# Kernel optimization log

Measured on AMD Instinct MI355X. Metric: run time of the kernel, lower is better.

## Reference

```python
import jax, jax.numpy as jnp
import numpy as np
import math

B, DIM, H, W = 4, 96, 64, 64
DIM3 = DIM * 3
DSTATE = 16

def _dwconv(x, w, b):
    # x: (B, d, L); torch Conv1d(k=4, pad=3, groups=d) then slice [:L] == left-pad 3
    y = jax.lax.conv_general_dilated(x, w, (1,), [(3, 0)],
                                     dimension_numbers=('NCH', 'OIH', 'NCH'),
                                     feature_group_count=x.shape[1])
    return y + b[None, :, None]

def _ln(x, g, b):
    m = jnp.mean(x, -1, keepdims=True)
    v = jnp.var(x, -1, keepdims=True)
    return (x - m) * jax.lax.rsqrt(v + 1e-5) * g + b

def _selective_scan(u, delta, A, Bs, Cs, D, z, delta_bias):
    # u, delta, z: (B, d, L); A: (d, N); Bs, Cs: (B, N, L)
    delta = jax.nn.softplus(delta + delta_bias[None, :, None])
    dT, uT = jnp.moveaxis(delta, 2, 0), jnp.moveaxis(u, 2, 0)   # (L, B, d)
    BT, CT = jnp.moveaxis(Bs, 2, 0), jnp.moveaxis(Cs, 2, 0)     # (L, B, N)
    h0 = jnp.zeros((u.shape[0], A.shape[0], A.shape[1]), u.dtype)
    def step(h, inp):
        d_t, u_t, b_t, c_t = inp
        h = jnp.exp(d_t[..., None] * A) * h + (d_t * u_t)[..., None] * b_t[:, None, :]
        return h, jnp.einsum('bdn,bn->bd', h, c_t)
    _, ys = jax.lax.scan(step, h0, (dT, uT, BT, CT))
    y = jnp.moveaxis(ys, 0, 2) + D[None, :, None] * u
    return y * jax.nn.silu(z)

def _sss(x, z_anchor, in_w, conv_w, conv_b, x_w, dt_w, dt_b, Alog, Dp, out_w):
    Bb, C, Hh, Ww = x.shape
    L = Hh * Ww
    r = dt_w.shape[0]
    xf = x.reshape(Bb, C, L).transpose(0, 2, 1) + z_anchor[:, None, :]
    x_in, z_gate = jnp.split(xf @ in_w, 2, axis=-1)
    xc = jax.nn.silu(_dwconv(x_in.transpose(0, 2, 1), conv_w, conv_b))  # (B, di, L)
    xdbl = xc.transpose(0, 2, 1) @ x_w
    dt, Bs, Cs = jnp.split(xdbl, [r, r + DSTATE], axis=-1)
    y = _selective_scan(xc, (dt @ dt_w).transpose(0, 2, 1), -jnp.exp(Alog),
                        Bs.transpose(0, 2, 1), Cs.transpose(0, 2, 1), Dp,
                        z_gate.transpose(0, 2, 1), dt_b)
    return (y.transpose(0, 2, 1) @ out_w).transpose(0, 2, 1).reshape(Bb, C, Hh, Ww)

def _sts(x, K, Q, in_w, conv_w, conv_b, kln_g, kln_b, k_w, k_b, qln_g, qln_b, q_w, q_b,
         dtbc_w, dt_w, dt_b, gate_w, gate_b, Alog, Dp, out_w):
    Bb, C, Hh, Ww = x.shape
    L = Hh * Ww
    r = dt_w.shape[0]
    xf = x.reshape(Bb, C, L).transpose(0, 2, 1)
    xc = jax.nn.silu(_dwconv((xf @ in_w).transpose(0, 2, 1), conv_w, conv_b))  # (B, di, L)
    x_t = xc.transpose(0, 2, 1)
    Kf = K.reshape(Bb, C, L).transpose(0, 2, 1)
    Qf = Q.reshape(Bb, C, L).transpose(0, 2, 1)
    K_p = jax.nn.silu(_ln(Kf, kln_g, kln_b) @ k_w + k_b)
    Q_p = jax.nn.silu(_ln(Qf, qln_g, qln_b) @ q_w + q_b)
    xdbl = jnp.concatenate([x_t, K_p], -1) @ dtbc_w
    dt, Bs, Cs = jnp.split(xdbl, [r, r + DSTATE], axis=-1)
    z_g = (jnp.concatenate([x_t, Q_p], -1) @ gate_w + gate_b).transpose(0, 2, 1)
    y = _selective_scan(xc, (dt @ dt_w).transpose(0, 2, 1), -jnp.exp(Alog),
                        Bs.transpose(0, 2, 1), Cs.transpose(0, 2, 1), Dp, z_g, dt_b)
    return (y.transpose(0, 2, 1) @ out_w).transpose(0, 2, 1).reshape(Bb, C, Hh, Ww)

def setup_inputs():
    key = jax.random.key(0)
    ks = iter(jax.random.split(key, 64))
    def nrm(shape, s=0.02):
        return jax.random.normal(next(ks), shape, jnp.float32) * s
    di, di3 = DIM * 2, DIM3 * 2
    r, r3 = math.ceil(DIM / 16), math.ceil(DIM3 / 16)
    Alog = jnp.log(jnp.tile(jnp.arange(1.0, DSTATE + 1.0, dtype=jnp.float32), (di, 1)))
    Alog3 = jnp.log(jnp.tile(jnp.arange(1.0, DSTATE + 1.0, dtype=jnp.float32), (di3, 1)))
    return dict(
        m_ll=jax.random.normal(next(ks), (B, DIM, H, W), jnp.float32),
        m_high=jax.random.normal(next(ks), (B, DIM3, H, W), jnp.float32),
        z=jax.random.normal(next(ks), (B, DIM), jnp.float32),
        K=jax.random.normal(next(ks), (B, DIM3, H, W), jnp.float32),
        Q=jax.random.normal(next(ks), (B, DIM3, H, W), jnp.float32),
        s_in_w=nrm((DIM, 2 * di)), s_conv_w=nrm((di, 1, 4), 0.2), s_conv_b=nrm((di,)),
        s_x_w=nrm((di, r + 2 * DSTATE)), s_dt_w=nrm((r, di)), s_dt_b=nrm((di,)),
        s_Alog=Alog, s_D=jnp.ones((di,), jnp.float32), s_out_w=nrm((di, DIM)),
        t_in_w=nrm((DIM3, di3)), t_conv_w=nrm((di3, 1, 4), 0.2), t_conv_b=nrm((di3,)),
        t_kln_g=jnp.ones((DIM3,), jnp.float32), t_kln_b=jnp.zeros((DIM3,), jnp.float32),
        t_k_w=nrm((DIM3, di3)), t_k_b=nrm((di3,)),
        t_qln_g=jnp.ones((DIM3,), jnp.float32), t_qln_b=jnp.zeros((DIM3,), jnp.float32),
        t_q_w=nrm((DIM3, di3)), t_q_b=nrm((di3,)),
        t_dtbc_w=nrm((2 * di3, r3 + 2 * DSTATE)), t_dt_w=nrm((r3, di3)), t_dt_b=nrm((di3,)),
        t_gate_w=nrm((2 * di3, di3)), t_gate_b=nrm((di3,)),
        t_Alog=Alog3, t_D=jnp.ones((di3,), jnp.float32), t_out_w=nrm((di3, DIM3)),
    )

def reference(m_ll, m_high, z, K, Q,
              s_in_w, s_conv_w, s_conv_b, s_x_w, s_dt_w, s_dt_b, s_Alog, s_D, s_out_w,
              t_in_w, t_conv_w, t_conv_b, t_kln_g, t_kln_b, t_k_w, t_k_b,
              t_qln_g, t_qln_b, t_q_w, t_q_b, t_dtbc_w, t_dt_w, t_dt_b,
              t_gate_w, t_gate_b, t_Alog, t_D, t_out_w):
    o1 = m_ll + _sss(m_ll, z, s_in_w, s_conv_w, s_conv_b, s_x_w, s_dt_w, s_dt_b, s_Alog, s_D, s_out_w)
    o2 = m_high + _sts(m_high, K, Q, t_in_w, t_conv_w, t_conv_b, t_kln_g, t_kln_b, t_k_w, t_k_b,
                       t_qln_g, t_qln_b, t_q_w, t_q_b, t_dtbc_w, t_dt_w, t_dt_b,
                       t_gate_w, t_gate_b, t_Alog, t_D, t_out_w)
    return (o1, o2)
```

## Files before the change

### kernel.cpp

```cpp
#include <hip/hip_runtime.h>
#include <math.h>

#define L 4096

typedef unsigned short u16;
typedef unsigned int u32;
typedef float f32x4 __attribute__((ext_vector_type(4)));
typedef short s16x8 __attribute__((ext_vector_type(8)));
typedef __attribute__((address_space(3))) unsigned int lds_u32;
typedef __attribute__((address_space(1))) unsigned int glb_u32;

__device__ __forceinline__ float softplus_f(float x) {
  return fmaxf(x, 0.f) + log1pf(__expf(-fabsf(x)));
}
__device__ __forceinline__ float silu_f(float x) {
  return x / (1.f + __expf(-x));
}
__device__ __forceinline__ float bf2f(u16 v) {
  return __uint_as_float(((unsigned)v) << 16);
}
__device__ __forceinline__ u16 f2bf(float f) {
  unsigned u = __float_as_uint(f);
  u += 0x7FFFu + ((u >> 16) & 1u);
  return (u16)(u >> 16);
}

struct WSeg { const float* src; u16* dst; int K, N, Npad; };
struct WAll { WSeg s[8]; };

__global__ __launch_bounds__(256) void wconv_k(WAll wa) {
  const WSeg w = wa.s[blockIdx.z];
  const int nb = blockIdx.x * 32, kb = blockIdx.y * 32;
  if (nb >= w.Npad || kb >= w.K) return;
  __shared__ float t[32][33];
  const int tx = threadIdx.x & 31, ty = threadIdx.x >> 5;
  for (int r = ty; r < 32; r += 8) {
    int k = kb + r, n = nb + tx;
    t[r][tx] = (n < w.N) ? w.src[(size_t)k * w.N + n] : 0.f;
  }
  __syncthreads();
  for (int r = ty; r < 32; r += 8) {
    int n = nb + r;
    w.dst[(size_t)n * w.K + kb + tx] = f2bf(t[tx][r]);
  }
}

struct TSeg { const float *x, *gam, *bet, *bias2; u16* out; int C, doLN; };
struct TPack { TSeg s[4]; };

__global__ __launch_bounds__(256) void trans_pack_k(TPack pk) {
  const TSeg t = pk.s[blockIdx.x >> 9];
  const int local = blockIdx.x & 511;
  const int C = t.C;
  __shared__ float tile[288][33];
  __shared__ float psum[8][32], psq[8][32];
  __shared__ float mm[32], rr[32];
  const int tid = threadIdx.x;
  const int l0 = (local & 127) * 32;
  const int b = local >> 7;
  const int lane32 = tid & 31, row8 = tid >> 5;
  const float* xb = t.x + (size_t)b * C * L + l0;

  for (int c = row8; c < C; c += 8)
    tile[c][lane32] = xb[(size_t)c * L + lane32];
  __syncthreads();

  if (t.doLN) {
    float s = 0.f, sq = 0.f;
    for (int c = row8; c < C; c += 8) {
      float v = tile[c][lane32];
      s += v; sq = fmaf(v, v, sq);
    }
    psum[row8][lane32] = s; psq[row8][lane32] = sq;
    __syncthreads();
    if (row8 == 0) {
      float ts = 0.f, tq = 0.f;
      #pragma unroll
      for (int g = 0; g < 8; ++g) { ts += psum[g][lane32]; tq += psq[g][lane32]; }
      float m = ts / C;
      float var = tq / C - m * m;
      mm[lane32] = m;
      rr[lane32] = rsqrtf(var + 1e-5f);
    }
    __syncthreads();
  }

  u16* ob = t.out + ((size_t)b * L + l0) * C;
  const int total = 32 * C;
  for (int o = tid * 8; o < total; o += 2048) {
    int tt = o / C, c = o % C;
    float m = 0.f, rs = 0.f;
    if (t.doLN) { m = mm[tt]; rs = rr[tt]; }
    union { u16 u[8]; int4 v; } pkv;
    #pragma unroll
    for (int j = 0; j < 8; ++j) {
      float v = tile[c + j][tt];
      if (t.doLN) v = (v - m) * rs * t.gam[c + j] + t.bet[c + j];
      else if (t.bias2) v += t.bias2[b * C + c + j];
      pkv.u[j] = f2bf(v);
    }
    *(int4*)(ob + o) = pkv.v;
  }
}

struct CSeg { const u16* x; const float* w; const float* b; u16* y; int C, nbx; };
struct CPack { CSeg s[2]; int start1; };

__global__ __launch_bounds__(256) void conv_pack_k(CPack pk) {
  const int bid = blockIdx.x;
  const int si = bid >= pk.start1;
  const CSeg q = pk.s[si];
  const int local = si ? bid - pk.start1 : bid;
  const int C = q.C;
  const int c = (local % q.nbx) * 64 + (threadIdx.x & 63);
  const int chunk = (local / q.nbx) * 4 + (threadIdx.x >> 6);
  const int T0 = chunk * 8;
  const float w0 = q.w[c * 4], w1 = q.w[c * 4 + 1], w2 = q.w[c * 4 + 2], w3 = q.w[c * 4 + 3];
  const float bs = q.b[c];
  const bool first = (T0 & (L - 1)) == 0;
  float v[11];
  #pragma unroll
  for (int i = 0; i < 11; ++i) {
    if (i < 3 && first) v[i] = 0.f;
    else v[i] = bf2f(q.x[(size_t)(T0 - 3 + i) * C + c]);
  }
  #pragma unroll
  for (int j = 0; j < 8; ++j) {
    float s = bs + w0 * v[j] + w1 * v[j + 1] + w2 * v[j + 2] + w3 * v[j + 3];
    q.y[(size_t)(T0 + j) * C + c] = f2bf(silu_f(s));
  }
}

struct MSeg {
  const u16 *A0, *A1, *Wt;
  const float *bias, *res;
  float* outF; u16 *outB0, *outB1;
  int K, K1, Nout, ldA, ldo, split, nbx, nwg, epi;
};
struct MPack { MSeg s[4]; int starts[4]; int nseg; };

__global__ __launch_bounds__(256) void mfma_pack_k(MPack pk) {
  const int bid = blockIdx.x;
  int si = 0;
  #pragma unroll
  for (int k = 1; k < 4; ++k)
    if (k < pk.nseg && bid >= pk.starts[k]) si = k;
  const MSeg p = pk.s[si];
  const int wg = bid - pk.starts[si];

  __shared__ u16 lds[16384];
  u16* As0 = lds;
  u16* Bs0 = lds + 8192;
  const int tid = threadIdx.x;
  const int lane = tid & 63;
  const int wid = tid >> 6;
  const int wm = wid >> 1, wn = wid & 1;
  const int newid = (wg & 7) * (p.nwg >> 3) + (wg >> 3);
  const int n0 = (newid % p.nbx) * 128;
  const int m0 = (newid / p.nbx) * 128;
  const int srow = tid & 127;
  const int skc = tid >> 7;
  const int kgrp = lane >> 4, l16 = lane & 15;

  f32x4 acc[4][4];
  #pragma unroll
  for (int i = 0; i < 4; ++i)
    #pragma unroll
    for (int j = 0; j < 4; ++j)
      acc[i][j] = (f32x4){0.f, 0.f, 0.f, 0.f};

  auto stage = [&](int bi, int k0) {
    const u16* Ab = p.A0;
    int kc = k0;
    if (p.A1 && k0 >= p.K1) { Ab = p.A1; kc = k0 - p.K1; }
    const u16* g0 = Ab + (size_t)(m0 + srow) * p.ldA + kc + skc * 8;
    u16* Ad = As0 + bi * 4096;
    __builtin_amdgcn_global_load_lds((const glb_u32*)g0,
        (lds_u32*)(Ad + wid * 512), 16, 0, 0);
    __builtin_amdgcn_global_load_lds((const glb_u32*)(g0 + 16),
        (lds_u32*)(Ad + 2048 + wid * 512), 16, 0, 0);
    const u16* h0 = p.Wt + (size_t)(n0 + srow) * p.K + k0 + skc * 8;
    u16* Bd = Bs0 + bi * 4096;
    __builtin_amdgcn_global_load_lds((const glb_u32*)h0,
        (lds_u32*)(Bd + wid * 512), 16, 0, 0);
    __builtin_amdgcn_global_load_lds((const glb_u32*)(h0 + 16),
        (lds_u32*)(Bd + 2048 + wid * 512), 16, 0, 0);
  };

  const int nt = p.K >> 5;
  stage(0, 0);
  __syncthreads();
  for (int t = 0; t < nt; ++t) {
    const int cur = t & 1;
    if (t + 1 < nt) stage(cur ^ 1, (t + 1) << 5);
    s16x8 af[4], bfr[4];
    #pragma unroll
    for (int mi = 0; mi < 4; ++mi)
      af[mi] = *(const s16x8*)(As0 + cur * 4096 + kgrp * 1024 + (wm * 64 + mi * 16 + l16) * 8);
    #pragma unroll
    for (int ni = 0; ni < 4; ++ni)
      bfr[ni] = *(const s16x8*)(Bs0 + cur * 4096 + kgrp * 1024 + (wn * 64 + ni * 16 + l16) * 8);
    #pragma unroll
    for (int mi = 0; mi < 4; ++mi)
      #pragma unroll
      for (int ni = 0; ni < 4; ++ni)
        acc[mi][ni] = __builtin_amdgcn_mfma_f32_16x16x32_bf16(af[mi], bfr[ni], acc[mi][ni], 0, 0, 0);
    if (t + 1 < nt) __syncthreads();
  }

  if (p.epi == 0) {
    #pragma unroll
    for (int mi = 0; mi < 4; ++mi) {
      #pragma unroll
      for (int j = 0; j < 4; ++j) {
        int token = m0 + wm * 64 + mi * 16 + (lane >> 4) * 4 + j;
        #pragma unroll
        for (int ni = 0; ni < 4; ++ni) {
          int n = n0 + wn * 64 + ni * 16 + l16;
          if (n < p.Nout) p.outF[(size_t)token * p.ldo + n] = acc[mi][ni][j];
        }
      }
    }
  } else if (p.epi == 2) {
    #pragma unroll
    for (int mi = 0; mi < 4; ++mi) {
      int token = m0 + wm * 64 + mi * 16 + (lane >> 4) * 4;
      int b = token >> 12, l = token & (L - 1);
      #pragma unroll
      for (int ni = 0; ni < 4; ++ni) {
        int n = n0 + wn * 64 + ni * 16 + l16;
        if (n < p.Nout) {
          size_t o = ((size_t)b * p.Nout + n) * L + l;
          float4 r = *(const float4*)(p.res + o);
          float4 v = make_float4(acc[mi][ni][0] + r.x, acc[mi][ni][1] + r.y,
                                 acc[mi][ni][2] + r.z, acc[mi][ni][3] + r.w);
          *(float4*)(p.outF + o) = v;
        }
      }
    }
  } else {
    __syncthreads();
    #pragma unroll
    for (int mi = 0; mi < 4; ++mi) {
      #pragma unroll
      for (int j = 0; j < 4; ++j) {
        int tok = wm * 64 + mi * 16 + (lane >> 4) * 4 + j;
        #pragma unroll
        for (int ni = 0; ni < 4; ++ni) {
          int nl = wn * 64 + ni * 16 + l16;
          int n = n0 + nl;
          float v = acc[mi][ni][j];
          if (n < p.Nout && (p.epi == 3 || p.epi == 4)) {
            v += p.bias[n];
            if (p.epi == 3) v = silu_f(v);
          }
          lds[tok * 128 + ((((nl >> 4) ^ (tok & 7))) << 4) + (nl & 15)] = f2bf(v);
        }
      }
    }
    __syncthreads();
    #pragma unroll
    for (int it = 0; it < 8; ++it) {
      int idx = it * 256 + tid;
      int row = idx >> 4, c16 = idx & 15;
      int nl0 = c16 * 8;
      if (n0 + nl0 < p.Nout) {
        int g = nl0 >> 4;
        int4 vv = *(const int4*)(lds + row * 128 + ((g ^ (row & 7)) << 4) + (nl0 & 15));
        int token = m0 + row;
        if (p.epi == 5) {
          int n = n0 + nl0;
          if (n < p.split) *(int4*)(p.outB0 + (size_t)token * p.split + n) = vv;
          else *(int4*)(p.outB1 + (size_t)token * p.split + (n - p.split)) = vv;
        } else {
          *(int4*)(p.outB0 + (size_t)token * p.ldo + n0 + nl0) = vv;
        }
      }
    }
  }
}

struct FSeg { const float* A0; const float* W; const float* eb; float* out; int K, N, lda, ldo, nbx; };
struct FPack { FSeg s[2]; int start1; };

__global__ __launch_bounds__(256) void gemm_f32_pack_k(FPack pk) {
  const int bid = blockIdx.x;
  const int si = bid >= pk.start1;
  const FSeg p = pk.s[si];
  const int local = si ? bid - pk.start1 : bid;
  const int n0 = (local % p.nbx) * 64;
  const int m0 = (local / p.nbx) * 64;

  __shared__ __align__(16) float As[16][64];
  __shared__ __align__(16) float Bs[16][64];
  const int tid = threadIdx.x;
  const int kidx = tid >> 4;
  const int li4 = (tid & 15) << 2;
  const int r0 = (tid & 15) << 2;
  const int c0 = (tid >> 4) << 2;
  float acc[4][4] = {};

  for (int k0 = 0; k0 < p.K; k0 += 16) {
    __syncthreads();
    {
      const int row = tid >> 2;
      const int kk4 = (tid & 3) << 2;
      const float* src = p.A0 + (size_t)(m0 + row) * p.lda;
      #pragma unroll
      for (int j = 0; j < 4; ++j) {
        int k = k0 + kk4 + j;
        As[kk4 + j][row] = (k < p.K) ? src[k] : 0.f;
      }
    }
    {
      int k = k0 + kidx;
      #pragma unroll
      for (int j = 0; j < 4; ++j) {
        int n = n0 + li4 + j;
        Bs[kidx][li4 + j] = (k < p.K && n < p.N) ? p.W[(size_t)k * p.N + n] : 0.f;
      }
    }
    __syncthreads();
    #pragma unroll
    for (int kk = 0; kk < 16; ++kk) {
      float4 a = *(const float4*)&As[kk][r0];
      float4 bq = *(const float4*)&Bs[kk][c0];
      float av[4] = {a.x, a.y, a.z, a.w};
      float bv[4] = {bq.x, bq.y, bq.z, bq.w};
      #pragma unroll
      for (int i = 0; i < 4; ++i)
        #pragma unroll
        for (int j = 0; j < 4; ++j)
          acc[i][j] = fmaf(av[i], bv[j], acc[i][j]);
    }
  }
  float eb[4] = {p.eb[n0 + c0], p.eb[n0 + c0 + 1], p.eb[n0 + c0 + 2], p.eb[n0 + c0 + 3]};
  #pragma unroll
  for (int i = 0; i < 4; ++i) {
    float4 v;
    v.x = softplus_f(acc[i][0] + eb[0]);
    v.y = softplus_f(acc[i][1] + eb[1]);
    v.z = softplus_f(acc[i][2] + eb[2]);
    v.w = softplus_f(acc[i][3] + eb[3]);
    *(float4*)&p.out[(size_t)(m0 + r0 + i) * p.ldo + n0 + c0] = v;
  }
}

struct S3Seg {
  const u16* u; const float* dlt; const float* Alog; const float* xdbl;
  const float* Dp; const u16* zT; float* PF; u16* yT;
  int roff, Dch, CLen, NCH, nsl;
};
struct S3Pack { S3Seg s[2]; int start1; };

template<int PASS>
__global__ __launch_bounds__(256) void scan3_pack_k(S3Pack pk) {
  __shared__ float rows[64][32];
  const int bid = blockIdx.x;
  const int si = bid >= pk.start1;
  const S3Seg q = pk.s[si];
  const int local = si ? bid - pk.start1 : bid;
  const int nsl = q.nsl;
  const int NC = L / q.CLen;
  const int slice = local % nsl;
  const int c = (local / nsl) % NC;
  const int b = local / (nsl * NC);
  const int tid = threadIdx.x;
  const size_t tok0 = (size_t)b * L + (size_t)c * q.CLen;

  const int W2 = (PASS == 1) ? 8 : 16;
  const int tot2 = q.CLen * W2;
  for (int i = tid; i < tot2; i += 256) {
    int r = i / W2, j = i - r * W2;
    float2 v = *(const float2*)(q.xdbl + (tok0 + r) * 64 + q.roff + 2 * j);
    *(float2*)&rows[r][2 * j] = v;
  }
  __syncthreads();

  if (tid < 192) {
    const int d = slice * 192 + tid;
    const int Dch = q.Dch;
    float An[16], h[16];
    #pragma unroll
    for (int n = 0; n < 16; ++n) {
      An[n] = -__expf(q.Alog[d * 16 + n]);
      h[n] = 0.f;
    }
    bool fast = true;
    #pragma unroll
    for (int n = 1; n < 16; ++n) {
      float ref = (float)(n + 1) * An[0];
      if (fabsf(An[n] - ref) > 1e-4f * fabsf(ref)) fast = false;
    }
    const int ch = b * Dch + d;
    if (PASS == 3) {
      #pragma unroll
      for (int n = 0; n < 16; ++n)
        h[n] = q.PF[((size_t)c * 32 + 16 + n) * q.NCH + ch];
    }
    const float Dd = q.Dp[d];
    const u16* up = q.u + tok0 * Dch + d;
    const float* dp = q.dlt + tok0 * Dch + d;
    const u16* zp = q.zT + tok0 * Dch + d;
    u16* yr = q.yT + tok0 * Dch + d;
    float S = 0.f;

    float dl_n = dp[0];
    float uu_n = bf2f(up[0]);
    float zv_n = (PASS == 3) ? bf2f(zp[0]) : 0.f;

    #define SCAN_BODY(FAST)                                                    \
    for (int t = 0; t < q.CLen; ++t) {                                         \
      float dl = dl_n, uu = uu_n, zv = zv_n;                                   \
      if (t + 1 < q.CLen) {                                                    \
        const size_t on = (size_t)(t + 1) * Dch;                               \
        dl_n = dp[on];                                                         \
        uu_n = bf2f(up[on]);                                                   \
        if (PASS == 3) zv_n = bf2f(zp[on]);                                    \
      }                                                                        \
      float w = dl * uu;                                                       \
      f32x4 B4[4];                                                             \
      _Pragma("unroll")                                                        \
      for (int g = 0; g < 4; ++g) B4[g] = *(const f32x4*)&rows[t][4 * g];      \
      if (PASS == 1) S += dl;                                                  \
      if (FAST) {                                                              \
        float a = __expf(dl * An[0]);                                          \
        float e[16];                                                           \
        e[0] = a;                                                              \
        e[1] = a * a;                                                          \
        e[2] = e[1] * e[0];                                                    \
        e[3] = e[1] * e[1];                                                    \
        e[4] = e[3] * e[0]; e[5] = e[3] * e[1];                                \
        e[6] = e[3] * e[2]; e[7] = e[3] * e[3];                                \
        _Pragma("unroll")                                                      \
        for (int j2 = 0; j2 < 8; ++j2) e[8 + j2] = e[7] * e[j2];               \
        _Pragma("unroll")                                                      \
        for (int n = 0; n < 16; ++n)                                           \
          h[n] = fmaf(e[n], h[n], w * B4[n >> 2][n & 3]);                      \
      } else {                                                                 \
        _Pragma("unroll")                                                      \
        for (int n = 0; n < 16; ++n)                                           \
          h[n] = fmaf(__expf(dl * An[n]), h[n], w * B4[n >> 2][n & 3]);        \
      }                                                                        \
      if (PASS == 3) {                                                         \
        f32x4 C4[4];                                                           \
        _Pragma("unroll")                                                      \
        for (int g = 0; g < 4; ++g) C4[g] = *(const f32x4*)&rows[t][16 + 4 * g]; \
        float y0 = 0.f, y1 = 0.f, y2 = 0.f, y3 = 0.f;                          \
        _Pragma("unroll")                                                      \
        for (int k2 = 0; k2 < 4; ++k2) {                                       \
          y0 = fmaf(h[k2],      C4[0][k2], y0);                                \
          y1 = fmaf(h[4 + k2],  C4[1][k2], y1);                                \
          y2 = fmaf(h[8 + k2],  C4[2][k2], y2);                                \
          y3 = fmaf(h[12 + k2], C4[3][k2], y3);                                \
        }                                                                      \
        float y = (y0 + y1) + (y2 + y3);                                       \
        yr[(size_t)t * Dch] = f2bf((y + Dd * uu) * silu_f(zv));                \
      }                                                                        \
    }

    if (fast) { SCAN_BODY(1) } else { SCAN_BODY(0) }
    #undef SCAN_BODY

    if (PASS == 1) {
      #pragma unroll
      for (int n = 0; n < 16; ++n) {
        q.PF[((size_t)c * 32 + n) * q.NCH + ch] = __expf(An[n] * S);
        q.PF[((size_t)c * 32 + 16 + n) * q.NCH + ch] = h[n];
      }
    }
  }
}

__global__ __launch_bounds__(256) void stitch_pack_k(
    float* PF0, int NC0, int NCH0, int tot0,
    float* PF1, int NC1, int NCH1, int tot1) {
  int idx = blockIdx.x * 256 + threadIdx.x;
  float* PF; int NC, NCH;
  if (idx < tot0) { PF = PF0; NC = NC0; NCH = NCH0; }
  else { idx -= tot0; if (idx >= tot1) return; PF = PF1; NC = NC1; NCH = NCH1; }
  int ch = idx % NCH, n = idx / NCH;
  float hin = 0.f;
  for (int c = 0; c < NC; ++c) {
    float* Ps = PF + ((size_t)c * 32 + n) * NCH + ch;
    float* Fs = PF + ((size_t)c * 32 + 16 + n) * NCH + ch;
    float Pv = *Ps, Fv = *Fs;
    *Fs = hin;
    hin = fmaf(Pv, hin, Fv);
  }
}

extern "C" void kernel_launch(void* const* d_in, const int* in_sizes, int n_in,
                              void* d_out, int out_size, void* d_ws, size_t ws_size,
                              hipStream_t stream) {
  const float* m_ll    = (const float*)d_in[0];
  const float* m_high  = (const float*)d_in[1];
  const float* zanc    = (const float*)d_in[2];
  const float* Kin     = (const float*)d_in[3];
  const float* Qin     = (const float*)d_in[4];
  const float* s_in_w  = (const float*)d_in[5];
  const float* s_conv_w= (const float*)d_in[6];
  const float* s_conv_b= (const float*)d_in[7];
  const float* s_x_w   = (const float*)d_in[8];
  const float* s_dt_w  = (const float*)d_in[9];
  const float* s_dt_b  = (const float*)d_in[10];
  const float* s_Alog  = (const float*)d_in[11];
  const float* s_D     = (const float*)d_in[12];
  const float* s_out_w = (const float*)d_in[13];
  const float* t_in_w  = (const float*)d_in[14];
  const float* t_conv_w= (const float*)d_in[15];
  const float* t_conv_b= (const float*)d_in[16];
  const float* t_kln_g = (const float*)d_in[17];
  const float* t_kln_b = (const float*)d_in[18];
  const float* t_k_w   = (const float*)d_in[19];
  const float* t_k_b   = (const float*)d_in[20];
  const float* t_qln_g = (const float*)d_in[21];
  const float* t_qln_b = (const float*)d_in[22];
  const float* t_q_w   = (const float*)d_in[23];
  const float* t_q_b   = (const float*)d_in[24];
  const float* t_dtbc_w= (const float*)d_in[25];
  const float* t_dt_w  = (const float*)d_in[26];
  const float* t_dt_b  = (const float*)d_in[27];
  const float* t_gate_w= (const float*)d_in[28];
  const float* t_gate_b= (const float*)d_in[29];
  const float* t_Alog  = (const float*)d_in[30];
  const float* t_D     = (const float*)d_in[31];
  const float* t_out_w = (const float*)d_in[32];

  float* out1 = (float*)d_out;
  float* out2 = out1 + (size_t)4 * 96 * L;
  float* ws = (float*)d_ws;

  u16* w_sin   = (u16*)(ws + 0);
  u16* w_sx    = (u16*)(ws + 18432);
  u16* w_sout  = (u16*)(ws + 30720);
  u16* w_tin   = (u16*)(ws + 43008);
  u16* w_tk    = (u16*)(ws + 135168);
  u16* w_tq    = (u16*)(ws + 227328);
  u16* w_tdtbc = (u16*)(ws + 319488);
  u16* w_tgate = (u16*)(ws + 393216);
  u16* w_tout  = (u16*)(ws + 761856);

  float* B_ahi  = ws + 872448;
  float* B_aK   = ws + 3231744;
  float* B_aQ   = ws + 5591040;
  float* B_all  = ws + 7950336;
  float* B_xin  = ws + 8736768;
  float* B_zTs  = ws + 10309632;
  float* B_xc   = ws + 11882496;
  float* B_xin3 = ws + 13455360;
  float* B_xc3  = ws + 18173952;
  float* B_kp   = ws + 22892544;
  float* B_qp   = ws + 27611136;
  float* B_zg3  = ws + 32329728;
  float* B_xdbl = ws + 37048320;
  float* B_xdbl3= ws + 38096896;
  float* B_PFs  = ws + 39145472;
  float* B_dlt  = B_ahi;
  float* B_dlt3 = B_kp;
  u16* y_bf = (u16*)B_xin;
  u16* y3   = (u16*)B_xin3;
  float* PFt = out2;

  dim3 blk(256);

  {
    WAll wa;
    wa.s[0] = {s_in_w,   w_sin,    96, 384, 384};
    wa.s[1] = {s_x_w,    w_sx,    192,  38, 128};
    wa.s[2] = {s_out_w,  w_sout,  192,  96, 128};
    wa.s[3] = {t_in_w,   w_tin,   288, 576, 640};
    wa.s[4] = {t_k_w,    w_tk,    288, 576, 640};
    wa.s[5] = {t_q_w,    w_tq,    288, 576, 640};
    wa.s[6] = {t_dtbc_w, w_tdtbc, 1152, 50, 128};
    wa.s[7] = {t_gate_w, w_tgate, 1152, 576, 640};
    wconv_k<<<dim3(20, 36, 8), blk, 0, stream>>>(wa);
    WAll wb;
    wb.s[0] = {t_out_w,  w_tout,  576, 288, 384};
    wconv_k<<<dim3(12, 18, 1), blk, 0, stream>>>(wb);
  }

  {
    TPack tp{};
    tp.s[0] = {m_ll,   nullptr, nullptr, zanc,    (u16*)B_all, 96,  0};
    tp.s[1] = {m_high, nullptr, nullptr, nullptr, (u16*)B_ahi, 288, 0};
    tp.s[2] = {Kin,    t_kln_g, t_kln_b, nullptr, (u16*)B_aK,  288, 1};
    tp.s[3] = {Qin,    t_qln_g, t_qln_b, nullptr, (u16*)B_aQ,  288, 1};
    trans_pack_k<<<dim3(2048), blk, 0, stream>>>(tp);
  }

  {
    MPack pk{}; pk.nseg = 4;
    pk.starts[0] = 0; pk.starts[1] = 384; pk.starts[2] = 1024; pk.starts[3] = 1664;
    MSeg a{}; a.A0 = (u16*)B_all; a.Wt = w_sin; a.K = 96; a.K1 = 1 << 28; a.Nout = 384;
    a.ldA = 96; a.split = 192; a.outB0 = (u16*)B_xin; a.outB1 = (u16*)B_zTs;
    a.nbx = 3; a.nwg = 384; a.epi = 5; pk.s[0] = a;
    MSeg b{}; b.A0 = (u16*)B_ahi; b.Wt = w_tin; b.K = 288; b.K1 = 1 << 28; b.Nout = 576;
    b.ldA = 288; b.ldo = 576; b.outB0 = (u16*)B_xin3; b.nbx = 5; b.nwg = 640; b.epi = 1; pk.s[1] = b;
    MSeg c{}; c.A0 = (u16*)B_aK; c.Wt = w_tk; c.K = 288; c.K1 = 1 << 28; c.Nout = 576;
    c.ldA = 288; c.ldo = 576; c.bias = t_k_b; c.outB0 = (u16*)B_kp; c.nbx = 5; c.nwg = 640; c.epi = 3; pk.s[2] = c;
    MSeg d{}; d.A0 = (u16*)B_aQ; d.Wt = w_tq; d.K = 288; d.K1 = 1 << 28; d.Nout = 576;
    d.ldA = 288; d.ldo = 576; d.bias = t_q_b; d.outB0 = (u16*)B_qp; d.nbx = 5; d.nwg = 640; d.epi = 3; pk.s[3] = d;
    mfma_pack_k<<<dim3(2304), blk, 0, stream>>>(pk);
  }

  {
    CPack cp{}; cp.start1 = 1536;
    cp.s[0] = {(u16*)B_xin,  s_conv_w, s_conv_b, (u16*)B_xc,  192, 3};
    cp.s[1] = {(u16*)B_xin3, t_conv_w, t_conv_b, (u16*)B_xc3, 576, 9};
    conv_pack_k<<<dim3(6144), blk, 0, stream>>>(cp);
  }

  {
    MPack pk{}; pk.nseg = 3;
    pk.starts[0] = 0; pk.starts[1] = 128; pk.starts[2] = 256; pk.starts[3] = 896;
    MSeg a{}; a.A0 = (u16*)B_xc; a.Wt = w_sx; a.K = 192; a.K1 = 1 << 28; a.Nout = 64;
    a.ldA = 192; a.ldo = 64; a.outF = B_xdbl; a.nbx = 1; a.nwg = 128; a.epi = 0; pk.s[0] = a;
    MSeg b{}; b.A0 = (u16*)B_xc3; b.A1 = (u16*)B_kp; b.Wt = w_tdtbc; b.K = 1152; b.K1 = 576;
    b.Nout = 64; b.ldA = 576; b.ldo = 64; b.outF = B_xdbl3; b.nbx = 1; b.nwg = 128; b.epi = 0; pk.s[1] = b;
    MSeg c{}; c.A0 = (u16*)B_xc3; c.A1 = (u16*)B_qp; c.Wt = w_tgate; c.K = 1152; c.K1 = 576;
    c.Nout = 576; c.ldA = 576; c.ldo = 576; c.bias = t_gate_b; c.outB0 = (u16*)B_zg3;
    c.nbx = 5; c.nwg = 640; c.epi = 4; pk.s[2] = c;
    mfma_pack_k<<<dim3(896), blk, 0, stream>>>(pk);
  }

  {
    FPack fp{}; fp.start1 = 768;
    fp.s[0] = {B_xdbl,  s_dt_w, s_dt_b, B_dlt,  6,  192, 64, 192, 3};
    fp.s[1] = {B_xdbl3, t_dt_w, t_dt_b, B_dlt3, 18, 576, 64, 576, 9};
    gemm_f32_pack_k<<<dim3(3072), blk, 0, stream>>>(fp);
  }

  S3Pack sp{}; sp.start1 = 512;
  sp.s[0] = {(u16*)B_xc,  B_dlt,  s_Alog, B_xdbl,  s_D, (u16*)B_zTs, B_PFs, y_bf, 6,  192, 32, 768,  1};
  sp.s[1] = {(u16*)B_xc3, B_dlt3, t_Alog, B_xdbl3, t_D, (u16*)B_zg3, PFt,   y3,   18, 576, 64, 2304, 3};
  scan3_pack_k<1><<<dim3(1280), blk, 0, stream>>>(sp);
  stitch_pack_k<<<dim3(192), blk, 0, stream>>>(B_PFs, 128, 768, 12288, PFt, 64, 2304, 36864);
  scan3_pack_k<3><<<dim3(1280), blk, 0, stream>>>(sp);

  {
    MPack pk{}; pk.nseg = 2;
    pk.starts[0] = 0; pk.starts[1] = 128; pk.starts[2] = 512; pk.starts[3] = 512;
    MSeg a{}; a.A0 = y_bf; a.Wt = w_sout; a.K = 192; a.K1 = 1 << 28; a.Nout = 96;
    a.ldA = 192; a.res = m_ll; a.outF = out1; a.nbx = 1; a.nwg = 128; a.epi = 2; pk.s[0] = a;
    MSeg b{}; b.A0 = y3; b.Wt = w_tout; b.K = 576; b.K1 = 1 << 28; b.Nout = 288;
    b.ldA = 576; b.res = m_high; b.outF = out2; b.nbx = 3; b.nwg = 384; b.epi = 2; pk.s[1] = b;
    mfma_pack_k<<<dim3(512), blk, 0, stream>>>(pk);
  }
}
```

Baseline: 408.8 us.

## Fuse dt projection and softplus into the selective scan kernels

Removes the separate fp32 GEMM that computed delta = softplus(dt @ dt_w + dt_b) into a full (tokens x channels) fp32 buffer. Each scan pass now stages the dt rows in LDS and recomputes delta per timestep with an 18-term dot product against per-thread weights held in registers. This removes one kernel launch plus the write and two reads of a large fp32 delta tensor. In exchange it adds register pressure and redundant arithmetic, since delta is computed in both scan passes.

```diff
diff --git a/kernel.cpp b/kernel.cpp
--- a/kernel.cpp
+++ b/kernel.cpp
@@ -280,82 +280,18 @@
   }
 }
 
-struct FSeg { const float* A0; const float* W; const float* eb; float* out; int K, N, lda, ldo, nbx; };
-struct FPack { FSeg s[2]; int start1; };
-
-__global__ __launch_bounds__(256) void gemm_f32_pack_k(FPack pk) {
-  const int bid = blockIdx.x;
-  const int si = bid >= pk.start1;
-  const FSeg p = pk.s[si];
-  const int local = si ? bid - pk.start1 : bid;
-  const int n0 = (local % p.nbx) * 64;
-  const int m0 = (local / p.nbx) * 64;
-
-  __shared__ __align__(16) float As[16][64];
-  __shared__ __align__(16) float Bs[16][64];
-  const int tid = threadIdx.x;
-  const int kidx = tid >> 4;
-  const int li4 = (tid & 15) << 2;
-  const int r0 = (tid & 15) << 2;
-  const int c0 = (tid >> 4) << 2;
-  float acc[4][4] = {};
-
-  for (int k0 = 0; k0 < p.K; k0 += 16) {
-    __syncthreads();
-    {
-      const int row = tid >> 2;
-      const int kk4 = (tid & 3) << 2;
-      const float* src = p.A0 + (size_t)(m0 + row) * p.lda;
-      #pragma unroll
-      for (int j = 0; j < 4; ++j) {
-        int k = k0 + kk4 + j;
-        As[kk4 + j][row] = (k < p.K) ? src[k] : 0.f;
-      }
-    }
-    {
-      int k = k0 + kidx;
-      #pragma unroll
-      for (int j = 0; j < 4; ++j) {
-        int n = n0 + li4 + j;
-        Bs[kidx][li4 + j] = (k < p.K && n < p.N) ? p.W[(size_t)k * p.N + n] : 0.f;
-      }
-    }
-    __syncthreads();
-    #pragma unroll
-    for (int kk = 0; kk < 16; ++kk) {
-      float4 a = *(const float4*)&As[kk][r0];
-      float4 bq = *(const float4*)&Bs[kk][c0];
-      float av[4] = {a.x, a.y, a.z, a.w};
-      float bv[4] = {bq.x, bq.y, bq.z, bq.w};
-      #pragma unroll
-      for (int i = 0; i < 4; ++i)
-        #pragma unroll
-        for (int j = 0; j < 4; ++j)
-          acc[i][j] = fmaf(av[i], bv[j], acc[i][j]);
-    }
-  }
-  float eb[4] = {p.eb[n0 + c0], p.eb[n0 + c0 + 1], p.eb[n0 + c0 + 2], p.eb[n0 + c0 + 3]};
-  #pragma unroll
-  for (int i = 0; i < 4; ++i) {
-    float4 v;
-    v.x = softplus_f(acc[i][0] + eb[0]);
-    v.y = softplus_f(acc[i][1] + eb[1]);
-    v.z = softplus_f(acc[i][2] + eb[2]);
-    v.w = softplus_f(acc[i][3] + eb[3]);
-    *(float4*)&p.out[(size_t)(m0 + r0 + i) * p.ldo + n0 + c0] = v;
-  }
-}
-
 struct S3Seg {
-  const u16* u; const float* dlt; const float* Alog; const float* xdbl;
+  const u16* u; const float* Alog; const float* xdbl;
+  const float* dtw; const float* dtb;
   const float* Dp; const u16* zT; float* PF; u16* yT;
-  int roff, Dch, CLen, NCH, nsl;
+  int rdim, Dch, CLen, NCH, nsl;
 };
 struct S3Pack { S3Seg s[2]; int start1; };
 
 template<int PASS>
 __global__ __launch_bounds__(256) void scan3_pack_k(S3Pack pk) {
-  __shared__ float rows[64][32];
+  __shared__ float rows_bc[64][32];
+  __shared__ float rows_dt[64][18];
   const int bid = blockIdx.x;
   const int si = bid >= pk.start1;
   const S3Seg q = pk.s[si];
@@ -368,12 +304,20 @@
   const int tid = threadIdx.x;
   const size_t tok0 = (size_t)b * L + (size_t)c * q.CLen;
 
-  const int W2 = (PASS == 1) ? 8 : 16;
-  const int tot2 = q.CLen * W2;
-  for (int i = tid; i < tot2; i += 256) {
-    int r = i / W2, j = i - r * W2;
-    float2 v = *(const float2*)(q.xdbl + (tok0 + r) * 64 + q.roff + 2 * j);
-    *(float2*)&rows[r][2 * j] = v;
+  {
+    const int W2 = (PASS == 1) ? 8 : 16;
+    const int tot2 = q.CLen * W2;
+    for (int i = tid; i < tot2; i += 256) {
+      int r = i / W2, j = i - r * W2;
+      float2 v = *(const float2*)(q.xdbl + (tok0 + r) * 64 + q.rdim + 2 * j);
+      *(float2*)&rows_bc[r][2 * j] = v;
+    }
+    const int totd = q.CLen * 9;
+    for (int i = tid; i < totd; i += 256) {
+      int r = i / 9, j = i - r * 9;
+      float2 v = *(const float2*)(q.xdbl + (tok0 + r) * 64 + 2 * j);
+      *(float2*)&rows_dt[r][2 * j] = v;
+    }
   }
   __syncthreads();
 
@@ -392,6 +336,12 @@
       float ref = (float)(n + 1) * An[0];
       if (fabsf(An[n] - ref) > 1e-4f * fabsf(ref)) fast = false;
     }
+    float wc[18];
+    #pragma unroll
+    for (int k = 0; k < 18; ++k)
+      wc[k] = (k < q.rdim) ? q.dtw[k * Dch + d] : 0.f;
+    const float db = q.dtb[d];
+
     const int ch = b * Dch + d;
     if (PASS == 3) {
       #pragma unroll
@@ -400,12 +350,21 @@
     }
     const float Dd = q.Dp[d];
     const u16* up = q.u + tok0 * Dch + d;
-    const float* dp = q.dlt + tok0 * Dch + d;
     const u16* zp = q.zT + tok0 * Dch + d;
     u16* yr = q.yT + tok0 * Dch + d;
     float S = 0.f;
 
-    float dl_n = dp[0];
+    auto dlt_at = [&](int t) {
+      float a0 = db, a1 = 0.f;
+      #pragma unroll
+      for (int k = 0; k < 9; ++k) {
+        a0 = fmaf(rows_dt[t][2 * k], wc[2 * k], a0);
+        a1 = fmaf(rows_dt[t][2 * k + 1], wc[2 * k + 1], a1);
+      }
+      return softplus_f(a0 + a1);
+    };
+
+    float dl_n = dlt_at(0);
     float uu_n = bf2f(up[0]);
     float zv_n = (PASS == 3) ? bf2f(zp[0]) : 0.f;
 
@@ -414,14 +373,14 @@
       float dl = dl_n, uu = uu_n, zv = zv_n;                                   \
       if (t + 1 < q.CLen) {                                                    \
         const size_t on = (size_t)(t + 1) * Dch;                               \
-        dl_n = dp[on];                                                         \
+        dl_n = dlt_at(t + 1);                                                  \
         uu_n = bf2f(up[on]);                                                   \
         if (PASS == 3) zv_n = bf2f(zp[on]);                                    \
       }                                                                        \
       float w = dl * uu;                                                       \
       f32x4 B4[4];                                                             \
       _Pragma("unroll")                                                        \
-      for (int g = 0; g < 4; ++g) B4[g] = *(const f32x4*)&rows[t][4 * g];      \
+      for (int g = 0; g < 4; ++g) B4[g] = *(const f32x4*)&rows_bc[t][4 * g];   \
       if (PASS == 1) S += dl;                                                  \
       if (FAST) {                                                              \
         float a = __expf(dl * An[0]);                                          \
@@ -445,7 +404,7 @@
       if (PASS == 3) {                                                         \
         f32x4 C4[4];                                                           \
         _Pragma("unroll")                                                      \
-        for (int g = 0; g < 4; ++g) C4[g] = *(const f32x4*)&rows[t][16 + 4 * g]; \
+        for (int g = 0; g < 4; ++g) C4[g] = *(const f32x4*)&rows_bc[t][16 + 4 * g]; \
         float y0 = 0.f, y1 = 0.f, y2 = 0.f, y3 = 0.f;                          \
         _Pragma("unroll")                                                      \
         for (int k2 = 0; k2 < 4; ++k2) {                                       \
@@ -556,8 +515,6 @@
   float* B_xdbl = ws + 37048320;
   float* B_xdbl3= ws + 38096896;
   float* B_PFs  = ws + 39145472;
-  float* B_dlt  = B_ahi;
-  float* B_dlt3 = B_kp;
   u16* y_bf = (u16*)B_xin;
   u16* y3   = (u16*)B_xin3;
   float* PFt = out2;
@@ -624,16 +581,9 @@
     mfma_pack_k<<<dim3(896), blk, 0, stream>>>(pk);
   }
 
-  {
-    FPack fp{}; fp.start1 = 768;
-    fp.s[0] = {B_xdbl,  s_dt_w, s_dt_b, B_dlt,  6,  192, 64, 192, 3};
-    fp.s[1] = {B_xdbl3, t_dt_w, t_dt_b, B_dlt3, 18, 576, 64, 576, 9};
-    gemm_f32_pack_k<<<dim3(3072), blk, 0, stream>>>(fp);
-  }
-
   S3Pack sp{}; sp.start1 = 512;
-  sp.s[0] = {(u16*)B_xc,  B_dlt,  s_Alog, B_xdbl,  s_D, (u16*)B_zTs, B_PFs, y_bf, 6,  192, 32, 768,  1};
-  sp.s[1] = {(u16*)B_xc3, B_dlt3, t_Alog, B_xdbl3, t_D, (u16*)B_zg3, PFt,   y3,   18, 576, 64, 2304, 3};
+  sp.s[0] = {(u16*)B_xc,  s_Alog, B_xdbl,  s_dt_w, s_dt_b, s_D, (u16*)B_zTs, B_PFs, y_bf, 6,  192, 32, 768,  1};
+  sp.s[1] = {(u16*)B_xc3, t_Alog, B_xdbl3, t_dt_w, t_dt_b, t_D, (u16*)B_zg3, PFt,   y3,   18, 576, 64, 2304, 3};
   scan3_pack_k<1><<<dim3(1280), blk, 0, stream>>>(sp);
   stitch_pack_k<<<dim3(192), blk, 0, stream>>>(B_PFs, 128, 768, 12288, PFt, 64, 2304, 36864);
   scan3_pack_k<3><<<dim3(1280), blk, 0, stream>>>(sp);
```

Result: slower. 445.9 us (+9.1%).
